# Performance work log

Measured on AMD Instinct MI355X. Metric: run time of the kernel, lower is better.

## Reference

```python
import jax, jax.numpy as jnp
import numpy as np

D_MODEL = 1024
D_STATE = 16
D_CONV = 4
EXPAND = 2
D_INNER = EXPAND * D_MODEL          # 2048
DT_RANK = (D_MODEL + 15) // 16      # 64
B_SZ, SEQ = 2, 1024
LN_EPS = 1e-6


def setup_inputs() -> dict:
    key = jax.random.key(0)
    ks = jax.random.split(key, 12)
    s = 0.02
    x = jax.random.normal(ks[0], (B_SZ, SEQ, D_MODEL), dtype=jnp.float32)
    W_in = jax.random.normal(ks[1], (D_MODEL, 2 * D_INNER), dtype=jnp.float32) * s
    conv_w = jax.random.normal(ks[2], (D_INNER, D_CONV), dtype=jnp.float32) * s
    conv_b = jnp.zeros((D_INNER,), dtype=jnp.float32)
    W_xproj = jax.random.normal(ks[3], (D_INNER, DT_RANK + 2 * D_STATE), dtype=jnp.float32) * s
    W_dt = jax.random.normal(ks[4], (DT_RANK, D_INNER), dtype=jnp.float32) * (DT_RANK ** -0.5)
    # dt bias ~ log-uniform init as in Mamba (softplus^-1 of dt in [1e-3, 1e-1])
    dt = jnp.exp(jax.random.uniform(ks[5], (D_INNER,)) * (np.log(0.1) - np.log(1e-3)) + np.log(1e-3))
    b_dt = dt + jnp.log(-jnp.expm1(-dt))  # inverse softplus
    A_log = jnp.log(jnp.broadcast_to(jnp.arange(1, D_STATE + 1, dtype=jnp.float32), (D_INNER, D_STATE)))
    D_param = jnp.ones((D_INNER,), dtype=jnp.float32)
    W_out = jax.random.normal(ks[6], (D_INNER, D_MODEL), dtype=jnp.float32) * s
    gamma = jnp.ones((D_MODEL,), dtype=jnp.float32)
    beta = jnp.zeros((D_MODEL,), dtype=jnp.float32)
    return {"x": x, "W_in": W_in, "conv_w": conv_w, "conv_b": conv_b,
            "W_xproj": W_xproj, "W_dt": W_dt, "b_dt": b_dt, "A_log": A_log,
            "D_param": D_param, "W_out": W_out, "gamma": gamma, "beta": beta}


def _mamba(x, W_in, conv_w, conv_b, W_xproj, W_dt, b_dt, A_log, D_param, W_out):
    B, L, _ = x.shape
    xz = x @ W_in                                  # [B,L,2*d_inner]
    xi, z = jnp.split(xz, 2, axis=-1)              # [B,L,d_inner] each
    # causal depthwise conv1d, kernel D_CONV
    xp = jnp.pad(xi, ((0, 0), (D_CONV - 1, 0), (0, 0)))
    xc = conv_b
    for k in range(D_CONV):
        xc = xc + xp[:, k:k + L, :] * conv_w[:, k]
    xc = jax.nn.silu(xc)                           # [B,L,d_inner]
    x_dbl = xc @ W_xproj                           # [B,L,dt_rank+2*d_state]
    dt_r = x_dbl[..., :DT_RANK]
    B_ssm = x_dbl[..., DT_RANK:DT_RANK + D_STATE]  # [B,L,d_state]
    C_ssm = x_dbl[..., DT_RANK + D_STATE:]         # [B,L,d_state]
    dt = jax.nn.softplus(dt_r @ W_dt + b_dt)       # [B,L,d_inner]
    A = -jnp.exp(A_log)                            # [d_inner,d_state]
    dA = jnp.exp(dt[..., None] * A)                # [B,L,d_inner,d_state]
    dBu = dt[..., None] * B_ssm[:, :, None, :] * xc[..., None]
    # selective scan over time (time-major for lax.scan)
    dA_t = jnp.moveaxis(dA, 1, 0)                  # [L,B,d_inner,d_state]
    dBu_t = jnp.moveaxis(dBu, 1, 0)
    C_t = jnp.moveaxis(C_ssm, 1, 0)                # [L,B,d_state]
    h0 = jnp.zeros((B, D_INNER, D_STATE), dtype=x.dtype)

    def step(h, inp):
        a, bu, c = inp
        h = a * h + bu
        y = jnp.einsum('bdn,bn->bd', h, c)
        return h, y

    _, ys = jax.lax.scan(step, h0, (dA_t, dBu_t, C_t))
    y = jnp.moveaxis(ys, 0, 1)                     # [B,L,d_inner]
    y = y + xc * D_param
    y = y * jax.nn.silu(z)
    return y @ W_out                               # [B,L,d_model]


def reference(x, W_in, conv_w, conv_b, W_xproj, W_dt, b_dt, A_log, D_param, W_out, gamma, beta):
    m = _mamba(x, W_in, conv_w, conv_b, W_xproj, W_dt, b_dt, A_log, D_param, W_out)
    mu = jnp.mean(m, axis=-1, keepdims=True)
    var = jnp.mean(jnp.square(m - mu), axis=-1, keepdims=True)
    ln = (m - mu) * jax.lax.rsqrt(var + LN_EPS) * gamma + beta
    return x + ln
```

## Files before the change

kernel.cpp:

```cpp
#include <hip/hip_runtime.h>
#include <math.h>

#define DM   1024
#define DI   2048
#define DS   16
#define DTR  64
#define NB   2
#define SEQL 1024
#define NTOK (NB*SEQL)
#define XND  96
#define XNP  128
#define CK   64
#define CL   16

typedef __bf16 bf16x8 __attribute__((ext_vector_type(8)));
typedef float  f32x4  __attribute__((ext_vector_type(4)));

#define PREP_BLOCKS 10624

__device__ inline void trans_tile(const float* __restrict__ W,
                                  __bf16* __restrict__ WT, int K, int N,
                                  int n0, int k0, int tid, __bf16 (*t)[33])
{
    const int tx = tid & 31, ty = tid >> 5;
    #pragma unroll
    for (int i = 0; i < 4; i++)
        t[ty * 4 + i][tx] = (__bf16)W[(size_t)(k0 + ty * 4 + i) * N + n0 + tx];
    __syncthreads();
    #pragma unroll
    for (int i = 0; i < 4; i++)
        WT[(size_t)(n0 + ty * 4 + i) * K + k0 + tx] = t[tx][ty * 4 + i];
}

__global__ __launch_bounds__(256) void prep(
    const float* __restrict__ x, const float* __restrict__ W_in,
    const float* __restrict__ W_out, const float* __restrict__ W_dt,
    const float* __restrict__ W_xprj,
    __bf16* __restrict__ xb, __bf16* __restrict__ W_inT,
    __bf16* __restrict__ W_outT, __bf16* __restrict__ WdtT,
    __bf16* __restrict__ W_xprT, float* __restrict__ xdbl,
    float* __restrict__ mbuf)
{
    __shared__ __bf16 t[32][33];
    int bid = blockIdx.x;
    const int tid = threadIdx.x;

    if (bid < 2304) {
        const int i = bid * 1024 + tid * 4;
        const float4 z = {0.f, 0.f, 0.f, 0.f};
        if (i < 262144) *reinterpret_cast<float4*>(&xdbl[i]) = z;
        else            *reinterpret_cast<float4*>(&mbuf[i - 262144]) = z;
        return;
    }
    bid -= 2304;
    if (bid < 1024) {
        const int e = (bid * 256 + tid) * 8;
        const float4 v0 = *reinterpret_cast<const float4*>(&x[e]);
        const float4 v1 = *reinterpret_cast<const float4*>(&x[e + 4]);
        bf16x8 o;
        o[0] = (__bf16)v0.x; o[1] = (__bf16)v0.y; o[2] = (__bf16)v0.z; o[3] = (__bf16)v0.w;
        o[4] = (__bf16)v1.x; o[5] = (__bf16)v1.y; o[6] = (__bf16)v1.z; o[7] = (__bf16)v1.w;
        *reinterpret_cast<bf16x8*>(&xb[e]) = o;
        return;
    }
    bid -= 1024;
    if (bid < 4096) {
        trans_tile(W_in, W_inT, DM, 2 * DI, (bid & 127) * 32, (bid >> 7) * 32, tid, t);
        return;
    }
    bid -= 4096;
    if (bid < 2048) {
        trans_tile(W_out, W_outT, DI, DM, (bid & 31) * 32, (bid >> 5) * 32, tid, t);
        return;
    }
    bid -= 2048;
    if (bid < 128) {
        trans_tile(W_dt, WdtT, DTR, DI, (bid & 63) * 32, (bid >> 6) * 32, tid, t);
        return;
    }
    bid -= 128;
    {
        const int idx = bid * 256 + tid;
        const int k = idx & (DI - 1);
        const int n = idx >> 11;
        W_xprT[(size_t)n * DI + k] = (n < XND) ? (__bf16)W_xprj[(size_t)k * XND + n]
                                               : (__bf16)0.f;
    }
}

template<int MODE>
__global__ __launch_bounds__(256) void gemm_bf16(
    const __bf16* __restrict__ A, const __bf16* __restrict__ Bt,
    void* __restrict__ Cp, int M, int N, int K, int ldc,
    const float* __restrict__ bias)
{
    __shared__ __bf16 As[128 * 64];
    __shared__ __bf16 Bs[128 * 64];
    const int tid  = threadIdx.x;
    const int lane = tid & 63;
    const int wid  = tid >> 6;
    const int wr   = wid >> 1, wc = wid & 1;
    const int brow = blockIdx.y * 128, bcol = blockIdx.x * 128;
    const int kper = K / gridDim.z;
    const int kbeg = blockIdx.z * kper, kend = kbeg + kper;

    f32x4 acc[4][4] = {};

    for (int k0 = kbeg; k0 < kend; k0 += 64) {
        __syncthreads();
        if (MODE == 2) {
            const float* Af = reinterpret_cast<const float*>(A);
            #pragma unroll
            for (int p = 0; p < 4; p++) {
                const int i = p * 256 + tid;
                const int r = i >> 3;
                const int j = i & 7;
                const float4 v0 = *reinterpret_cast<const float4*>(
                    &Af[(size_t)(brow + r) * XNP + j * 8]);
                const float4 v1 = *reinterpret_cast<const float4*>(
                    &Af[(size_t)(brow + r) * XNP + j * 8 + 4]);
                bf16x8 o;
                o[0] = (__bf16)v0.x; o[1] = (__bf16)v0.y; o[2] = (__bf16)v0.z; o[3] = (__bf16)v0.w;
                o[4] = (__bf16)v1.x; o[5] = (__bf16)v1.y; o[6] = (__bf16)v1.z; o[7] = (__bf16)v1.w;
                *reinterpret_cast<bf16x8*>(&As[r * 64 + ((j ^ (r & 7))) * 8]) = o;
            }
        } else {
            #pragma unroll
            for (int p = 0; p < 4; p++) {
                const int i = p * 256 + tid;
                const int r = i >> 3;
                const int gc = ((i & 7) ^ (r & 7)) * 8;
                __builtin_amdgcn_global_load_lds(
                    (const __attribute__((address_space(1))) void*)(A + (size_t)(brow + r) * K + k0 + gc),
                    (__attribute__((address_space(3))) void*)(As + i * 8), 16, 0, 0);
            }
        }
        #pragma unroll
        for (int p = 0; p < 4; p++) {
            const int i = p * 256 + tid;
            const int r = i >> 3;
            const int gc = ((i & 7) ^ (r & 7)) * 8;
            __builtin_amdgcn_global_load_lds(
                (const __attribute__((address_space(1))) void*)(Bt + (size_t)(bcol + r) * K + k0 + gc),
                (__attribute__((address_space(3))) void*)(Bs + i * 8), 16, 0, 0);
        }
        __syncthreads();
        bf16x8 a[2][4], b[2][4];
        const int rA = wr * 64 + (lane & 15);
        const int rB = wc * 64 + (lane & 15);
        const int cq = lane >> 4;
        const int rx = lane & 7;
        #pragma unroll
        for (int ks = 0; ks < 2; ks++) {
            const int sl = ((ks * 4 + cq) ^ rx) * 8;
            #pragma unroll
            for (int m = 0; m < 4; m++) {
                a[ks][m] = *reinterpret_cast<const bf16x8*>(&As[(rA + m * 16) * 64 + sl]);
                b[ks][m] = *reinterpret_cast<const bf16x8*>(&Bs[(rB + m * 16) * 64 + sl]);
            }
        }
        #pragma unroll
        for (int ks = 0; ks < 2; ks++)
            #pragma unroll
            for (int m = 0; m < 4; m++)
                #pragma unroll
                for (int n = 0; n < 4; n++)
                    acc[m][n] = __builtin_amdgcn_mfma_f32_16x16x32_bf16(
                        a[ks][m], b[ks][n], acc[m][n], 0, 0, 0);
    }
    const int crow = brow + wr * 64 + (lane >> 4) * 4;
    const int ccol = bcol + wc * 64 + (lane & 15);
    #pragma unroll
    for (int m = 0; m < 4; m++)
        #pragma unroll
        for (int n = 0; n < 4; n++) {
            const int col = ccol + n * 16;
            #pragma unroll
            for (int j = 0; j < 4; j++) {
                const size_t idx = (size_t)(crow + m * 16 + j) * ldc + col;
                if (MODE == 0) {
                    ((float*)Cp)[idx] = acc[m][n][j];
                } else if (MODE == 1) {
                    atomicAdd(&((float*)Cp)[idx], acc[m][n][j]);
                } else if (MODE == 2) {
                    const float v = acc[m][n][j] + bias[col];
                    ((__bf16*)Cp)[idx] =
                        (__bf16)(fmaxf(v, 0.f) + log1pf(__expf(-fabsf(v))));
                } else {
                    ((__bf16*)Cp)[idx] = (__bf16)acc[m][n][j];
                }
            }
        }
}

__global__ __launch_bounds__(256) void conv_silu(
    const __bf16* __restrict__ xzb, const float* __restrict__ conv_w,
    const float* __restrict__ conv_b, __bf16* __restrict__ xcb)
{
    const int g  = blockIdx.x * 256 + threadIdx.x;
    const int d0 = (g & 255) * 8;
    const int tok = g >> 8;
    const int t   = tok & (SEQL - 1);

    float4 wv[8];
    #pragma unroll
    for (int j = 0; j < 8; j++)
        wv[j] = *reinterpret_cast<const float4*>(&conv_w[(d0 + j) * 4]);
    float acc[8];
    {
        const float4 b0 = *reinterpret_cast<const float4*>(&conv_b[d0]);
        const float4 b1 = *reinterpret_cast<const float4*>(&conv_b[d0 + 4]);
        acc[0] = b0.x; acc[1] = b0.y; acc[2] = b0.z; acc[3] = b0.w;
        acc[4] = b1.x; acc[5] = b1.y; acc[6] = b1.z; acc[7] = b1.w;
    }
    #pragma unroll
    for (int k = 0; k < 4; k++) {
        const int tt = t + k - 3;
        if (tt >= 0) {
            const bf16x8 v = *reinterpret_cast<const bf16x8*>(
                &xzb[(size_t)(tok + k - 3) * (2 * DI) + d0]);
            #pragma unroll
            for (int j = 0; j < 8; j++) {
                const float wk = (k == 0) ? wv[j].x : (k == 1) ? wv[j].y
                               : (k == 2) ? wv[j].z : wv[j].w;
                acc[j] += (float)v[j] * wk;
            }
        }
    }
    bf16x8 o;
    #pragma unroll
    for (int j = 0; j < 8; j++) {
        const float a = acc[j];
        o[j] = (__bf16)(a / (1.f + __expf(-a)));
    }
    *reinterpret_cast<bf16x8*>(&xcb[(size_t)g * 8]) = o;
}

__global__ __launch_bounds__(256) void scan_partial(
    const __bf16* __restrict__ xcb, const float* __restrict__ xdbl,
    const __bf16* __restrict__ dtb, const float* __restrict__ A_log,
    float* __restrict__ hpart, float* __restrict__ sdtb)
{
    __shared__ float Bsh[CL][16];
    const int tid = threadIdx.x;
    const int d = blockIdx.x * 256 + tid;
    const int c = blockIdx.y, b = blockIdx.z;
    const size_t base = (size_t)b * SEQL + c * CL;
    {
        const int st = tid >> 4, sg = tid & 15;
        Bsh[st][sg] = xdbl[(base + st) * XNP + DTR + sg];
    }
    float dtv[CL], xcv[CL];
    #pragma unroll
    for (int t = 0; t < CL; t++) {
        dtv[t] = (float)dtb[(base + t) * DI + d];
        xcv[t] = (float)xcb[(base + t) * DI + d];
    }
    float Av[16];
    #pragma unroll
    for (int i = 0; i < 4; i++) {
        const float4 v = *reinterpret_cast<const float4*>(&A_log[(size_t)d * 16 + i * 4]);
        Av[i*4+0] = -__expf(v.x); Av[i*4+1] = -__expf(v.y);
        Av[i*4+2] = -__expf(v.z); Av[i*4+3] = -__expf(v.w);
    }
    __syncthreads();
    float h[16] = {};
    float sdt = 0.f;
    #pragma unroll
    for (int t = 0; t < CL; t++) {
        sdt += dtv[t];
        const float dx = dtv[t] * xcv[t];
        #pragma unroll
        for (int n = 0; n < 16; n++)
            h[n] = __expf(dtv[t] * Av[n]) * h[n] + dx * Bsh[t][n];
    }
    const size_t ob = ((size_t)(b * CK + c) * DI + d) * 16;
    #pragma unroll
    for (int i = 0; i < 4; i++) {
        float4 v; v.x = h[i*4]; v.y = h[i*4+1]; v.z = h[i*4+2]; v.w = h[i*4+3];
        *reinterpret_cast<float4*>(&hpart[ob + i * 4]) = v;
    }
    sdtb[(size_t)(b * CK + c) * DI + d] = sdt;
}

__global__ __launch_bounds__(256) void scan_combine(
    const float* __restrict__ A_log, const float* __restrict__ sdtb,
    const float* __restrict__ hpart, float* __restrict__ hentry)
{
    const int idx = blockIdx.x * 256 + threadIdx.x;
    const int n = idx & 15;
    const int d = (idx >> 4) & (DI - 1);
    const int b = idx >> 15;
    const float A = -__expf(A_log[(size_t)d * 16 + n]);
    float h = 0.f;
    #pragma unroll
    for (int cb = 0; cb < CK / 16; cb++) {
        float hl[16], sv[16];
        #pragma unroll
        for (int j = 0; j < 16; j++) {
            const int c = cb * 16 + j;
            hl[j] = hpart[((size_t)(b * CK + c) * DI + d) * 16 + n];
            sv[j] = sdtb[(size_t)(b * CK + c) * DI + d];
        }
        #pragma unroll
        for (int j = 0; j < 16; j++) {
            const int c = cb * 16 + j;
            hentry[((size_t)(b * CK + c) * DI + d) * 16 + n] = h;
            h = __expf(A * sv[j]) * h + hl[j];
        }
    }
}

__global__ __launch_bounds__(256) void scan_final(
    const __bf16* __restrict__ xzb, const __bf16* __restrict__ xcb,
    const float* __restrict__ xdbl, const __bf16* __restrict__ dtb,
    const float* __restrict__ A_log, const float* __restrict__ Dp,
    const float* __restrict__ hentry, __bf16* __restrict__ yb)
{
    __shared__ float Bsh[CL][16];
    __shared__ float Csh[CL][16];
    const int tid = threadIdx.x;
    const int d = blockIdx.x * 256 + tid;
    const int c = blockIdx.y, b = blockIdx.z;
    const size_t base = (size_t)b * SEQL + c * CL;
    {
        const int st = tid >> 4, sg = tid & 15;
        Bsh[st][sg] = xdbl[(base + st) * XNP + DTR + sg];
        Csh[st][sg] = xdbl[(base + st) * XNP + DTR + DS + sg];
    }
    float dtv[CL], xcv[CL], zv[CL];
    #pragma unroll
    for (int t = 0; t < CL; t++) {
        dtv[t] = (float)dtb[(base + t) * DI + d];
        xcv[t] = (float)xcb[(base + t) * DI + d];
        zv[t]  = (float)xzb[(base + t) * (2 * DI) + DI + d];
    }
    float Av[16];
    #pragma unroll
    for (int i = 0; i < 4; i++) {
        const float4 v = *reinterpret_cast<const float4*>(&A_log[(size_t)d * 16 + i * 4]);
        Av[i*4+0] = -__expf(v.x); Av[i*4+1] = -__expf(v.y);
        Av[i*4+2] = -__expf(v.z); Av[i*4+3] = -__expf(v.w);
    }
    float h[16];
    const size_t ob = ((size_t)(b * CK + c) * DI + d) * 16;
    #pragma unroll
    for (int i = 0; i < 4; i++) {
        const float4 v = *reinterpret_cast<const float4*>(&hentry[ob + i * 4]);
        h[i*4] = v.x; h[i*4+1] = v.y; h[i*4+2] = v.z; h[i*4+3] = v.w;
    }
    const float Dv = Dp[d];
    __syncthreads();
    #pragma unroll
    for (int t = 0; t < CL; t++) {
        const float dx = dtv[t] * xcv[t];
        float y = 0.f;
        #pragma unroll
        for (int n = 0; n < 16; n++) {
            h[n] = __expf(dtv[t] * Av[n]) * h[n] + dx * Bsh[t][n];
            y += h[n] * Csh[t][n];
        }
        y += xcv[t] * Dv;
        y *= zv[t] / (1.f + __expf(-zv[t]));
        yb[(base + t) * DI + d] = (__bf16)y;
    }
}

__global__ __launch_bounds__(256) void ln_add(
    const float* __restrict__ x, const float* __restrict__ m,
    const float* __restrict__ gamma, const float* __restrict__ beta,
    float* __restrict__ out)
{
    const int tok = blockIdx.x;
    const int tid = threadIdx.x;
    const int lane = tid & 63, wave = tid >> 6;
    __shared__ float red[4];
    __shared__ float stats[2];

    const float4 v = reinterpret_cast<const float4*>(&m[(size_t)tok * DM])[tid];
    float s = v.x + v.y + v.z + v.w;
    #pragma unroll
    for (int o = 32; o > 0; o >>= 1) s += __shfl_down(s, o, 64);
    if (lane == 0) red[wave] = s;
    __syncthreads();
    if (tid == 0) stats[0] = (red[0] + red[1] + red[2] + red[3]) * (1.f / DM);
    __syncthreads();
    const float mu = stats[0];
    const float dx = v.x - mu, dy = v.y - mu, dz = v.z - mu, dw = v.w - mu;
    float q = dx * dx + dy * dy + dz * dz + dw * dw;
    #pragma unroll
    for (int o = 32; o > 0; o >>= 1) q += __shfl_down(q, o, 64);
    if (lane == 0) red[wave] = q;
    __syncthreads();
    if (tid == 0)
        stats[1] = rsqrtf((red[0] + red[1] + red[2] + red[3]) * (1.f / DM) + 1e-6f);
    __syncthreads();
    const float rs = stats[1];

    const float4 g  = reinterpret_cast<const float4*>(gamma)[tid];
    const float4 bb = reinterpret_cast<const float4*>(beta)[tid];
    const float4 xv = reinterpret_cast<const float4*>(&x[(size_t)tok * DM])[tid];
    float4 o;
    o.x = xv.x + dx * rs * g.x + bb.x;
    o.y = xv.y + dy * rs * g.y + bb.y;
    o.z = xv.z + dz * rs * g.z + bb.z;
    o.w = xv.w + dw * rs * g.w + bb.w;
    reinterpret_cast<float4*>(&out[(size_t)tok * DM])[tid] = o;
}

extern "C" void kernel_launch(void* const* d_in, const int* in_sizes, int n_in,
                              void* d_out, int out_size, void* d_ws, size_t ws_size,
                              hipStream_t stream)
{
    const float* x      = (const float*)d_in[0];
    const float* W_in   = (const float*)d_in[1];
    const float* conv_w = (const float*)d_in[2];
    const float* conv_b = (const float*)d_in[3];
    const float* W_xprj = (const float*)d_in[4];
    const float* W_dt   = (const float*)d_in[5];
    const float* b_dt   = (const float*)d_in[6];
    const float* A_log  = (const float*)d_in[7];
    const float* D_par  = (const float*)d_in[8];
    const float* W_out  = (const float*)d_in[9];
    const float* gamma  = (const float*)d_in[10];
    const float* beta   = (const float*)d_in[11];
    float* out = (float*)d_out;

    char* w = (char*)d_ws;
    __bf16* xzb    = (__bf16*)(w + 0);
    __bf16* xcb    = (__bf16*)(w + 16777216);
    float*  xdbl   = (float*) (w + 25165824);
    __bf16* dtb    = (__bf16*)(w + 26214400);
    float*  mbuf   = (float*) (w + 34603008);
    float*  hpart  = (float*) (w + 42991616);
    float*  sdtb   = (float*) (w + 59768832);
    __bf16* xb     = (__bf16*)(w + 60817408);
    __bf16* W_inT  = (__bf16*)(w + 65011712);
    __bf16* W_outT = (__bf16*)(w + 73400320);
    __bf16* W_xprT = (__bf16*)(w + 77594624);
    __bf16* WdtT   = (__bf16*)(w + 78118912);
    __bf16* yb     = (__bf16*)(w + 78381056);
    float*  hentry = (float*) (w + 86769664);

    prep<<<PREP_BLOCKS, 256, 0, stream>>>(
        x, W_in, W_out, W_dt, W_xprj, xb, W_inT, W_outT, WdtT, W_xprT, xdbl, mbuf);

    gemm_bf16<3><<<dim3(32, 16, 1), 256, 0, stream>>>(
        xb, W_inT, xzb, NTOK, 2 * DI, DM, 2 * DI, nullptr);

    conv_silu<<<(NTOK * DI / 8) / 256, 256, 0, stream>>>(xzb, conv_w, conv_b, xcb);

    gemm_bf16<1><<<dim3(1, 16, 16), 256, 0, stream>>>(
        xcb, W_xprT, xdbl, NTOK, XNP, DI, XNP, nullptr);

    gemm_bf16<2><<<dim3(16, 16, 1), 256, 0, stream>>>(
        (const __bf16*)xdbl, WdtT, dtb, NTOK, DI, DTR, DI, b_dt);

    scan_partial<<<dim3(DI / 256, CK, NB), 256, 0, stream>>>(
        xcb, xdbl, dtb, A_log, hpart, sdtb);
    scan_combine<<<NB * DI * DS / 256, 256, 0, stream>>>(A_log, sdtb, hpart, hentry);
    scan_final<<<dim3(DI / 256, CK, NB), 256, 0, stream>>>(
        xzb, xcb, xdbl, dtb, A_log, D_par, hentry, yb);

    gemm_bf16<1><<<dim3(8, 16, 4), 256, 0, stream>>>(
        yb, W_outT, mbuf, NTOK, DM, DI, DM, nullptr);

    ln_add<<<NTOK, 256, 0, stream>>>(x, mbuf, gamma, beta, out);
}
```

Measured before the change: 185.2 us.

## Double-buffer GEMM LDS tiles and add XCD-aware block swizzle

The shared bf16 GEMM now uses two LDS buffers per operand, so the next K-tile's global-to-LDS loads are issued while MFMAs run on the current tile, with one barrier per iteration instead of two. A templated block-index remap spreads consecutive linear block IDs across groups of eight and is applied to the in-projection and out-projection GEMMs to improve cache locality across chiplets. LDS use per block doubles to 64 KB, which can cut occupancy. Correctness depends on the global_load_lds writes having completed at the barrier without an explicit vmcnt wait.

```diff
diff --git a/kernel.cpp b/kernel.cpp
--- a/kernel.cpp
+++ b/kernel.cpp
@@ -88,26 +88,36 @@
     }
 }
 
-template<int MODE>
+template<int MODE, int SWZ>
 __global__ __launch_bounds__(256) void gemm_bf16(
     const __bf16* __restrict__ A, const __bf16* __restrict__ Bt,
     void* __restrict__ Cp, int M, int N, int K, int ldc,
     const float* __restrict__ bias)
 {
-    __shared__ __bf16 As[128 * 64];
-    __shared__ __bf16 Bs[128 * 64];
+    __shared__ __bf16 As[2][128 * 64];
+    __shared__ __bf16 Bs[2][128 * 64];
     const int tid  = threadIdx.x;
     const int lane = tid & 63;
     const int wid  = tid >> 6;
     const int wr   = wid >> 1, wc = wid & 1;
-    const int brow = blockIdx.y * 128, bcol = blockIdx.x * 128;
+
+    int bx = blockIdx.x, by = blockIdx.y;
+    if (SWZ != 0) {
+        const int gx = gridDim.x, gy = gridDim.y;
+        const int nxy = gx * gy;
+        const int q = nxy >> 3;
+        int lin = by * gx + bx;
+        lin = (lin & 7) * q + (lin >> 3);
+        if (SWZ == 1) { by = lin / gx; bx = lin % gx; }
+        else          { bx = lin / gy; by = lin % gy; }
+    }
+    const int brow = by * 128, bcol = bx * 128;
     const int kper = K / gridDim.z;
     const int kbeg = blockIdx.z * kper, kend = kbeg + kper;
 
     f32x4 acc[4][4] = {};
 
-    for (int k0 = kbeg; k0 < kend; k0 += 64) {
-        __syncthreads();
+    auto stage = [&](int buf, int k0) {
         if (MODE == 2) {
             const float* Af = reinterpret_cast<const float*>(A);
             #pragma unroll
@@ -122,7 +132,7 @@
                 bf16x8 o;
                 o[0] = (__bf16)v0.x; o[1] = (__bf16)v0.y; o[2] = (__bf16)v0.z; o[3] = (__bf16)v0.w;
                 o[4] = (__bf16)v1.x; o[5] = (__bf16)v1.y; o[6] = (__bf16)v1.z; o[7] = (__bf16)v1.w;
-                *reinterpret_cast<bf16x8*>(&As[r * 64 + ((j ^ (r & 7))) * 8]) = o;
+                *reinterpret_cast<bf16x8*>(&As[buf][r * 64 + ((j ^ (r & 7))) * 8]) = o;
             }
         } else {
             #pragma unroll
@@ -132,7 +142,7 @@
                 const int gc = ((i & 7) ^ (r & 7)) * 8;
                 __builtin_amdgcn_global_load_lds(
                     (const __attribute__((address_space(1))) void*)(A + (size_t)(brow + r) * K + k0 + gc),
-                    (__attribute__((address_space(3))) void*)(As + i * 8), 16, 0, 0);
+                    (__attribute__((address_space(3))) void*)(&As[buf][i * 8]), 16, 0, 0);
             }
         }
         #pragma unroll
@@ -142,9 +152,18 @@
             const int gc = ((i & 7) ^ (r & 7)) * 8;
             __builtin_amdgcn_global_load_lds(
                 (const __attribute__((address_space(1))) void*)(Bt + (size_t)(bcol + r) * K + k0 + gc),
-                (__attribute__((address_space(3))) void*)(Bs + i * 8), 16, 0, 0);
-        }
-        __syncthreads();
+                (__attribute__((address_space(3))) void*)(&Bs[buf][i * 8]), 16, 0, 0);
+        }
+    };
+
+    const int nt = (kend - kbeg) >> 6;
+    stage(0, kbeg);
+    __syncthreads();
+    int cur = 0;
+    for (int t = 0; t < nt; t++) {
+        if (t + 1 < nt) stage(cur ^ 1, kbeg + ((t + 1) << 6));
+        const __bf16* Ab = &As[cur][0];
+        const __bf16* Bb = &Bs[cur][0];
         bf16x8 a[2][4], b[2][4];
         const int rA = wr * 64 + (lane & 15);
         const int rB = wc * 64 + (lane & 15);
@@ -155,8 +174,8 @@
             const int sl = ((ks * 4 + cq) ^ rx) * 8;
             #pragma unroll
             for (int m = 0; m < 4; m++) {
-                a[ks][m] = *reinterpret_cast<const bf16x8*>(&As[(rA + m * 16) * 64 + sl]);
-                b[ks][m] = *reinterpret_cast<const bf16x8*>(&Bs[(rB + m * 16) * 64 + sl]);
+                a[ks][m] = *reinterpret_cast<const bf16x8*>(&Ab[(rA + m * 16) * 64 + sl]);
+                b[ks][m] = *reinterpret_cast<const bf16x8*>(&Bb[(rB + m * 16) * 64 + sl]);
             }
         }
         #pragma unroll
@@ -167,6 +186,8 @@
                 for (int n = 0; n < 4; n++)
                     acc[m][n] = __builtin_amdgcn_mfma_f32_16x16x32_bf16(
                         a[ks][m], b[ks][n], acc[m][n], 0, 0, 0);
+        __syncthreads();
+        cur ^= 1;
     }
     const int crow = brow + wr * 64 + (lane >> 4) * 4;
     const int ccol = bcol + wc * 64 + (lane & 15);
@@ -445,15 +466,15 @@
     prep<<<PREP_BLOCKS, 256, 0, stream>>>(
         x, W_in, W_out, W_dt, W_xprj, xb, W_inT, W_outT, WdtT, W_xprT, xdbl, mbuf);
 
-    gemm_bf16<3><<<dim3(32, 16, 1), 256, 0, stream>>>(
+    gemm_bf16<3, 2><<<dim3(32, 16, 1), 256, 0, stream>>>(
         xb, W_inT, xzb, NTOK, 2 * DI, DM, 2 * DI, nullptr);
 
     conv_silu<<<(NTOK * DI / 8) / 256, 256, 0, stream>>>(xzb, conv_w, conv_b, xcb);
 
-    gemm_bf16<1><<<dim3(1, 16, 16), 256, 0, stream>>>(
+    gemm_bf16<1, 0><<<dim3(1, 16, 16), 256, 0, stream>>>(
         xcb, W_xprT, xdbl, NTOK, XNP, DI, XNP, nullptr);
 
-    gemm_bf16<2><<<dim3(16, 16, 1), 256, 0, stream>>>(
+    gemm_bf16<2, 0><<<dim3(16, 16, 1), 256, 0, stream>>>(
         (const __bf16*)xdbl, WdtT, dtb, NTOK, DI, DTR, DI, b_dt);
 
     scan_partial<<<dim3(DI / 256, CK, NB), 256, 0, stream>>>(
@@ -462,7 +483,7 @@
     scan_final<<<dim3(DI / 256, CK, NB), 256, 0, stream>>>(
         xzb, xcb, xdbl, dtb, A_log, D_par, hentry, yb);
 
-    gemm_bf16<1><<<dim3(8, 16, 4), 256, 0, stream>>>(
+    gemm_bf16<1, 1><<<dim3(8, 16, 4), 256, 0, stream>>>(
         yb, W_outT, mbuf, NTOK, DM, DI, DM, nullptr);
 
     ln_add<<<NTOK, 256, 0, stream>>>(x, mbuf, gamma, beta, out);
```

Result: no change. 183.5 us (-0.9%).
